# Kernel tuning notes

Measured on AMD Instinct MI355X. Metric: run time of the kernel, lower is better.

The kernel has to match this reference:

```python
import jax, jax.numpy as jnp
import numpy as np

N_LAT, N_LON = 721, 1440
N_MESH = 40962
C_IN, N_FEAT = 64, 4
HID, OUT = 256, 256
BATCH = 2


def _precompute_interp(mesh_lat, mesh_lon):
    """Vectorized version of BilinearInterpolator.__init__ precompute."""
    lat_min, lon_min = -np.pi / 2, 0.0
    dlat = np.pi / (N_LAT - 1)
    dlon = 2 * np.pi / N_LON
    lon = np.mod(mesh_lon - lon_min, 2 * np.pi) + lon_min
    lat_idx = (mesh_lat - lat_min) / dlat
    lon_idx = (lon - lon_min) / dlon
    i0 = np.clip(np.floor(lat_idx).astype(np.int64), 0, N_LAT - 2)
    j0 = np.clip(np.floor(lon_idx).astype(np.int64), 0, N_LON - 2)
    i1 = i0 + 1
    j1 = (j0 + 1) % N_LON
    lf = np.clip(lat_idx - i0, 0.0, 1.0)
    jf = np.clip(lon_idx - j0, 0.0, 1.0)
    idx = np.stack([i0 * N_LON + j0, i0 * N_LON + j1,
                    i1 * N_LON + j0, i1 * N_LON + j1], axis=1)
    w = np.stack([(1 - lf) * (1 - jf), (1 - lf) * jf,
                  lf * (1 - jf), lf * jf], axis=1).astype(np.float32)
    return idx, w


def setup_inputs() -> dict:
    key = jax.random.key(0)
    k = jax.random.split(key, 6)
    rng = np.random.default_rng(0)
    mesh_lat = rng.uniform(-np.pi / 2 + 1e-3, np.pi / 2 - 1e-3, N_MESH)
    mesh_lon = rng.uniform(0.0, 2 * np.pi, N_MESH)
    idx, w = _precompute_interp(mesh_lat, mesh_lon)
    d_in = C_IN + N_FEAT
    return {
        "grid_data": jax.random.normal(k[0], (BATCH, N_LAT, N_LON, C_IN), jnp.float32),
        "mesh_features": jax.random.normal(k[1], (N_MESH, N_FEAT), jnp.float32),
        "indices": jnp.asarray(idx, jnp.int64 if jax.config.read('jax_enable_x64') else jnp.int32),
        "weights": jnp.asarray(w),
        "W1": jax.random.normal(k[2], (d_in, HID), jnp.float32) / np.sqrt(d_in),
        "b1": jnp.zeros((HID,), jnp.float32),
        "W2": jax.random.normal(k[3], (HID, OUT), jnp.float32) / np.sqrt(HID),
        "b2": jnp.zeros((OUT,), jnp.float32),
    }


def reference(grid_data, mesh_features, indices, weights, W1, b1, W2, b2):
    B, n_lat, n_lon, C = grid_data.shape
    grid_flat = grid_data.reshape(B, n_lat * n_lon, C)          # (B, G, C)
    corner = grid_flat[:, indices, :]                           # (B, M, 4, C)
    mesh_data = jnp.einsum('bmkc,mk->bmc', corner, weights)     # weighted 4-pt sum
    mf = jnp.broadcast_to(mesh_features[None], (B,) + mesh_features.shape)
    combined = jnp.concatenate([mesh_data, mf], axis=-1)        # (B, M, C+F)
    h = jax.nn.relu(combined @ W1 + b1)                         # 2-layer MLP
    return h @ W2 + b2                                          # (B, M, OUT)
```

## Files before the change

kernel.cpp:

```cpp
#include <hip/hip_runtime.h>
#include <hip/hip_bf16.h>


constexpr int kNLat  = 721;
constexpr int kNLon  = 1440;
constexpr long long kNPix = (long long)kNLat * kNLon;
constexpr int kMesh  = 40962;
constexpr int kCIn   = 64;
constexpr int kFeat  = 4;
constexpr int kDIn   = kCIn + kFeat;
constexpr int kHid   = 256;
constexpr int kOut   = 256;
constexpr int kBatch = 2;

constexpr int kPts    = kBatch * kMesh;
constexpr int kPtsPad = (kPts + 63) & ~63;

typedef __attribute__((ext_vector_type(8))) short bf16x8;
typedef __attribute__((ext_vector_type(4))) float f32x4;

constexpr int    WSA1_N   = 16 * 3 * 64 * 8;
constexpr int    WSB2_N   = 16 * 8 * 64 * 8;
constexpr size_t WS_BYTES = (size_t)(WSA1_N + WSB2_N) * 2;

constexpr int MP    = 64;
constexpr int NBLKB = kPtsPad / MP;
constexpr int CSTR  = 128;
constexpr int HSTR  = 256;

__device__ inline ushort f2b(float v) {
    __hip_bfloat16 h = __float2bfloat16(v);
    return *reinterpret_cast<ushort*>(&h);
}

__device__ inline int cswz(int r, int c) { return r * CSTR + (c ^ ((r & 7) << 3)); }
__device__ inline int hswz(int r, int c) { return r * HSTR + (c ^ ((r & 7) << 3)); }

__global__ __launch_bounds__(256)
void g2m_prep(const float* __restrict__ W1, const float* __restrict__ W2,
              ushort* __restrict__ ws) {
    const int tid = blockIdx.x * 256 + threadIdx.x;
    if (tid < 3072) {
        const int l  = tid & 63;
        const int g  = tid >> 6;
        const int ks = g % 3;
        const int rt = g / 3;
        const int hid = rt * 16 + (l & 15);
        const int k0  = ks * 32 + (l >> 4) * 8;
        ushort tmp[8];
        #pragma unroll
        for (int j = 0; j < 8; ++j) {
            const int k = k0 + j;
            tmp[j] = f2b(k < kDIn ? W1[(size_t)k * kHid + hid] : 0.f);
        }
        *reinterpret_cast<bf16x8*>(ws + (size_t)tid * 8) =
            *reinterpret_cast<bf16x8*>(tmp);
    } else if (tid < 11264) {
        const int q  = tid - 3072;
        const int l  = q & 63;
        const int g  = q >> 6;
        const int ks = g % 8;
        const int ct = g / 8;
        const int col = ct * 16 + (l & 15);
        const int k0  = ks * 32 + (l >> 4) * 8;
        ushort tmp[8];
        #pragma unroll
        for (int j = 0; j < 8; ++j) {
            const int k = k0 + j;
            tmp[j] = f2b(W2[(size_t)k * kOut + col]);
        }
        *reinterpret_cast<bf16x8*>(ws + (size_t)(WSA1_N + q * 8)) =
            *reinterpret_cast<bf16x8*>(tmp);
    }
}

__global__ __launch_bounds__(256, 3)
void g2m_fused3(const float* __restrict__ grid,
                const float* __restrict__ mfeat,
                const int*   __restrict__ indices,
                const float* __restrict__ weights,
                const float* __restrict__ b1,
                const float* __restrict__ b2,
                const ushort* __restrict__ ws,
                float* __restrict__ out)
{
    __shared__ __align__(16) ushort comb[MP * CSTR];
    __shared__ __align__(16) ushort hbuf[MP * HSTR];

    const int t    = threadIdx.x;
    const int lane = t & 63;
    const int w    = t >> 6;
    const int p0   = blockIdx.x * MP;
    const int l15  = lane & 15;
    const int l4   = lane >> 4;

    {
        const int q = l4;
        float4 rr[4][4];
        float4 wtv[4];
        float  mf0[4], mf1[4];

        #pragma unroll
        for (int it = 0; it < 4; ++it) {
            const int p = p0 + w * 16 + it * 4 + q;
            rr[it][0] = rr[it][1] = rr[it][2] = rr[it][3] = float4{0.f, 0.f, 0.f, 0.f};
            wtv[it] = float4{0.f, 0.f, 0.f, 0.f};
            mf0[it] = 0.f; mf1[it] = 0.f;
            if (p < kPts) {
                const int b = (p >= kMesh) ? 1 : 0;
                const int m = p - b * kMesh;
                const int4 id = *reinterpret_cast<const int4*>(indices + (size_t)m * 4);
                wtv[it] = *reinterpret_cast<const float4*>(weights + (size_t)m * 4);
                const float* gb = grid + (size_t)b * (size_t)(kNPix * kCIn);
                rr[it][0] = *reinterpret_cast<const float4*>(gb + (size_t)id.x * kCIn + l15 * 4);
                rr[it][1] = *reinterpret_cast<const float4*>(gb + (size_t)id.y * kCIn + l15 * 4);
                rr[it][2] = *reinterpret_cast<const float4*>(gb + (size_t)id.z * kCIn + l15 * 4);
                rr[it][3] = *reinterpret_cast<const float4*>(gb + (size_t)id.w * kCIn + l15 * 4);
                if (l15 < 2) {
                    mf0[it] = mfeat[(size_t)m * kFeat + l15 * 2];
                    mf1[it] = mfeat[(size_t)m * kFeat + l15 * 2 + 1];
                }
            }
        }

        #pragma unroll
        for (int it = 0; it < 4; ++it) {
            const int row = w * 16 + it * 4 + q;
            const float4 wt = wtv[it];
            float4 acc;
            acc.x = fmaf(wt.x, rr[it][0].x, fmaf(wt.y, rr[it][1].x, fmaf(wt.z, rr[it][2].x, wt.w * rr[it][3].x)));
            acc.y = fmaf(wt.x, rr[it][0].y, fmaf(wt.y, rr[it][1].y, fmaf(wt.z, rr[it][2].y, wt.w * rr[it][3].y)));
            acc.z = fmaf(wt.x, rr[it][0].z, fmaf(wt.y, rr[it][1].z, fmaf(wt.z, rr[it][2].z, wt.w * rr[it][3].z)));
            acc.w = fmaf(wt.x, rr[it][0].w, fmaf(wt.y, rr[it][1].w, fmaf(wt.z, rr[it][2].w, wt.w * rr[it][3].w)));
            ushort4 pk;
            pk.x = f2b(acc.x); pk.y = f2b(acc.y); pk.z = f2b(acc.z); pk.w = f2b(acc.w);
            *reinterpret_cast<ushort4*>(&comb[cswz(row, l15 * 4)]) = pk;
            ushort2 ft;
            ft.x = f2b(mf0[it]); ft.y = f2b(mf1[it]);
            *reinterpret_cast<ushort2*>(&comb[cswz(row, 64 + l15 * 2)]) = ft;
        }
    }
    __syncthreads();

    {
        f32x4 acc1[4][4];
        #pragma unroll
        for (int r = 0; r < 4; ++r)
            #pragma unroll
            for (int mt = 0; mt < 4; ++mt) acc1[r][mt] = (f32x4)0.f;

        #pragma unroll
        for (int ks = 0; ks < 3; ++ks) {
            bf16x8 af[4], bfr[4];
            #pragma unroll
            for (int r = 0; r < 4; ++r) {
                const int rt = w * 4 + r;
                af[r] = *reinterpret_cast<const bf16x8*>(
                            ws + (size_t)((rt * 3 + ks) * 64 + lane) * 8);
            }
            #pragma unroll
            for (int mt = 0; mt < 4; ++mt)
                bfr[mt] = *reinterpret_cast<const bf16x8*>(
                            &comb[cswz(mt * 16 + l15, ks * 32 + l4 * 8)]);
            #pragma unroll
            for (int r = 0; r < 4; ++r)
                #pragma unroll
                for (int mt = 0; mt < 4; ++mt)
                    acc1[r][mt] = __builtin_amdgcn_mfma_f32_16x16x32_bf16(
                                      af[r], bfr[mt], acc1[r][mt], 0, 0, 0);
        }

        #pragma unroll
        for (int r = 0; r < 4; ++r) {
            const int hid0 = (w * 4 + r) * 16 + l4 * 4;
            const float4 bv = *reinterpret_cast<const float4*>(b1 + hid0);
            #pragma unroll
            for (int mt = 0; mt < 4; ++mt) {
                const int m = mt * 16 + l15;
                ushort4 hv;
                hv.x = f2b(fmaxf(acc1[r][mt][0] + bv.x, 0.f));
                hv.y = f2b(fmaxf(acc1[r][mt][1] + bv.y, 0.f));
                hv.z = f2b(fmaxf(acc1[r][mt][2] + bv.z, 0.f));
                hv.w = f2b(fmaxf(acc1[r][mt][3] + bv.w, 0.f));
                *reinterpret_cast<ushort4*>(&hbuf[hswz(m, hid0)]) = hv;
            }
        }
    }
    __syncthreads();

    {
        f32x4 acc2[4][4];
        #pragma unroll
        for (int mt = 0; mt < 4; ++mt)
            #pragma unroll
            for (int c = 0; c < 4; ++c) acc2[mt][c] = (f32x4)0.f;

        #pragma unroll
        for (int ks = 0; ks < 8; ++ks) {
            bf16x8 hf[4], wf[4];
            #pragma unroll
            for (int mt = 0; mt < 4; ++mt)
                hf[mt] = *reinterpret_cast<const bf16x8*>(
                            &hbuf[hswz(mt * 16 + l15, ks * 32 + l4 * 8)]);
            #pragma unroll
            for (int c = 0; c < 4; ++c) {
                const int ct = w * 4 + c;
                wf[c] = *reinterpret_cast<const bf16x8*>(
                            ws + (size_t)(WSA1_N + ((ct * 8 + ks) * 64 + lane) * 8));
            }
            #pragma unroll
            for (int mt = 0; mt < 4; ++mt)
                #pragma unroll
                for (int c = 0; c < 4; ++c)
                    acc2[mt][c] = __builtin_amdgcn_mfma_f32_16x16x32_bf16(
                                      wf[c], hf[mt], acc2[mt][c], 0, 0, 0);
        }

        #pragma unroll
        for (int c = 0; c < 4; ++c) {
            const int col0 = (w * 4 + c) * 16 + l4 * 4;
            const float4 bv = *reinterpret_cast<const float4*>(b2 + col0);
            #pragma unroll
            for (int mt = 0; mt < 4; ++mt) {
                const int p = p0 + mt * 16 + l15;
                if (p < kPts) {
                    float4 o;
                    o.x = acc2[mt][c][0] + bv.x;
                    o.y = acc2[mt][c][1] + bv.y;
                    o.z = acc2[mt][c][2] + bv.z;
                    o.w = acc2[mt][c][3] + bv.w;
                    *reinterpret_cast<float4*>(out + (size_t)p * kOut + col0) = o;
                }
            }
        }
    }
}

extern "C" void kernel_launch(void* const* d_in, const int* in_sizes, int n_in,
                              void* d_out, int out_size, void* d_ws, size_t ws_size,
                              hipStream_t stream) {
    const float* grid    = (const float*)d_in[0];
    const float* mfeat   = (const float*)d_in[1];
    const int*   indices = (const int*)d_in[2];
    const float* weights = (const float*)d_in[3];
    const float* W1      = (const float*)d_in[4];
    const float* b1      = (const float*)d_in[5];
    const float* W2      = (const float*)d_in[6];
    const float* b2      = (const float*)d_in[7];
    float* o = (float*)d_out;

    if (ws_size >= WS_BYTES) {
        ushort* ws = (ushort*)d_ws;
        g2m_prep<<<44, 256, 0, stream>>>(W1, W2, ws);
        g2m_fused3<<<NBLKB, 256, 0, stream>>>(grid, mfeat, indices, weights,
                                              b1, b2, ws, o);
    }
}
```

Before: 52.88 us.

## Process two point tiles per block, prefetching second gather during first MLP

Each block now handles two 64-point tiles. It loads the index, weight and feature metadata for both tiles up front, then issues the grid-row gather for the second tile while the first tile's two MFMA GEMMs run. A second LDS staging buffer holds the second tile's combined input, and occupancy is lowered from 3 to 2 blocks per CU with half as many blocks launched. The goal is to hide gather latency behind the matrix work. The cost is much higher register pressure from holding a second tile's gathered rows, which could cause spills, plus lower occupancy and an uneven tail across CUs.

```diff
diff --git a/kernel.cpp b/kernel.cpp
--- a/kernel.cpp
+++ b/kernel.cpp
@@ -24,7 +24,7 @@
 constexpr size_t WS_BYTES = (size_t)(WSA1_N + WSB2_N) * 2;
 
 constexpr int MP    = 64;
-constexpr int NBLKB = kPtsPad / MP;
+constexpr int NBLK2 = (kPtsPad + 2 * MP - 1) / (2 * MP);
 constexpr int CSTR  = 128;
 constexpr int HSTR  = 256;
 
@@ -74,8 +74,177 @@
     }
 }
 
-__global__ __launch_bounds__(256, 3)
-void g2m_fused3(const float* __restrict__ grid,
+struct GRegs {
+    float4 rr[4][4];
+    float4 wt[4];
+    float  mf0[4], mf1[4];
+};
+
+__device__ inline void load_meta(const int* __restrict__ indices,
+                                 const float* __restrict__ weights,
+                                 const float* __restrict__ mfeat,
+                                 int p0, int w, int l15, int l4,
+                                 int4 (&id)[4], GRegs& g) {
+    #pragma unroll
+    for (int it = 0; it < 4; ++it) {
+        const int p = p0 + w * 16 + it * 4 + l4;
+        id[it] = int4{0, 0, 0, 0};
+        g.wt[it] = float4{0.f, 0.f, 0.f, 0.f};
+        g.mf0[it] = 0.f; g.mf1[it] = 0.f;
+        if (p < kPts) {
+            const int b = (p >= kMesh) ? 1 : 0;
+            const int m = p - b * kMesh;
+            id[it] = *reinterpret_cast<const int4*>(indices + (size_t)m * 4);
+            id[it].x += b ? (int)kNPix : 0;
+            id[it].y += b ? (int)kNPix : 0;
+            id[it].z += b ? (int)kNPix : 0;
+            id[it].w += b ? (int)kNPix : 0;
+            g.wt[it] = *reinterpret_cast<const float4*>(weights + (size_t)m * 4);
+            if (l15 < 2) {
+                g.mf0[it] = mfeat[(size_t)m * kFeat + l15 * 2];
+                g.mf1[it] = mfeat[(size_t)m * kFeat + l15 * 2 + 1];
+            }
+        }
+    }
+}
+
+__device__ inline void load_rows(const float* __restrict__ grid,
+                                 int p0, int w, int l15, int l4,
+                                 const int4 (&id)[4], GRegs& g) {
+    #pragma unroll
+    for (int it = 0; it < 4; ++it) {
+        const int p = p0 + w * 16 + it * 4 + l4;
+        g.rr[it][0] = g.rr[it][1] = g.rr[it][2] = g.rr[it][3] = float4{0.f, 0.f, 0.f, 0.f};
+        if (p < kPts) {
+            g.rr[it][0] = *reinterpret_cast<const float4*>(grid + (size_t)id[it].x * kCIn + l15 * 4);
+            g.rr[it][1] = *reinterpret_cast<const float4*>(grid + (size_t)id[it].y * kCIn + l15 * 4);
+            g.rr[it][2] = *reinterpret_cast<const float4*>(grid + (size_t)id[it].z * kCIn + l15 * 4);
+            g.rr[it][3] = *reinterpret_cast<const float4*>(grid + (size_t)id[it].w * kCIn + l15 * 4);
+        }
+    }
+}
+
+__device__ inline void reduce_tile(const GRegs& g, ushort* comb,
+                                   int w, int l15, int l4) {
+    #pragma unroll
+    for (int it = 0; it < 4; ++it) {
+        const int row = w * 16 + it * 4 + l4;
+        const float4 wt = g.wt[it];
+        float4 acc;
+        acc.x = fmaf(wt.x, g.rr[it][0].x, fmaf(wt.y, g.rr[it][1].x, fmaf(wt.z, g.rr[it][2].x, wt.w * g.rr[it][3].x)));
+        acc.y = fmaf(wt.x, g.rr[it][0].y, fmaf(wt.y, g.rr[it][1].y, fmaf(wt.z, g.rr[it][2].y, wt.w * g.rr[it][3].y)));
+        acc.z = fmaf(wt.x, g.rr[it][0].z, fmaf(wt.y, g.rr[it][1].z, fmaf(wt.z, g.rr[it][2].z, wt.w * g.rr[it][3].z)));
+        acc.w = fmaf(wt.x, g.rr[it][0].w, fmaf(wt.y, g.rr[it][1].w, fmaf(wt.z, g.rr[it][2].w, wt.w * g.rr[it][3].w)));
+        ushort4 pk;
+        pk.x = f2b(acc.x); pk.y = f2b(acc.y); pk.z = f2b(acc.z); pk.w = f2b(acc.w);
+        *reinterpret_cast<ushort4*>(&comb[cswz(row, l15 * 4)]) = pk;
+        ushort2 ft;
+        ft.x = f2b(g.mf0[it]); ft.y = f2b(g.mf1[it]);
+        *reinterpret_cast<ushort2*>(&comb[cswz(row, 64 + l15 * 2)]) = ft;
+    }
+}
+
+__device__ inline void gemm1(const ushort* comb, ushort* hbuf,
+                             const ushort* __restrict__ ws,
+                             const float* __restrict__ b1,
+                             int w, int lane, int l15, int l4) {
+    f32x4 acc1[4][4];
+    #pragma unroll
+    for (int r = 0; r < 4; ++r)
+        #pragma unroll
+        for (int mt = 0; mt < 4; ++mt) acc1[r][mt] = (f32x4)0.f;
+
+    #pragma unroll
+    for (int ks = 0; ks < 3; ++ks) {
+        bf16x8 af[4], bfr[4];
+        #pragma unroll
+        for (int r = 0; r < 4; ++r) {
+            const int rt = w * 4 + r;
+            af[r] = *reinterpret_cast<const bf16x8*>(
+                        ws + (size_t)((rt * 3 + ks) * 64 + lane) * 8);
+        }
+        #pragma unroll
+        for (int mt = 0; mt < 4; ++mt)
+            bfr[mt] = *reinterpret_cast<const bf16x8*>(
+                        &comb[cswz(mt * 16 + l15, ks * 32 + l4 * 8)]);
+        #pragma unroll
+        for (int r = 0; r < 4; ++r)
+            #pragma unroll
+            for (int mt = 0; mt < 4; ++mt)
+                acc1[r][mt] = __builtin_amdgcn_mfma_f32_16x16x32_bf16(
+                                  af[r], bfr[mt], acc1[r][mt], 0, 0, 0);
+    }
+
+    #pragma unroll
+    for (int r = 0; r < 4; ++r) {
+        const int hid0 = (w * 4 + r) * 16 + l4 * 4;
+        const float4 bv = *reinterpret_cast<const float4*>(b1 + hid0);
+        #pragma unroll
+        for (int mt = 0; mt < 4; ++mt) {
+            const int m = mt * 16 + l15;
+            ushort4 hv;
+            hv.x = f2b(fmaxf(acc1[r][mt][0] + bv.x, 0.f));
+            hv.y = f2b(fmaxf(acc1[r][mt][1] + bv.y, 0.f));
+            hv.z = f2b(fmaxf(acc1[r][mt][2] + bv.z, 0.f));
+            hv.w = f2b(fmaxf(acc1[r][mt][3] + bv.w, 0.f));
+            *reinterpret_cast<ushort4*>(&hbuf[hswz(m, hid0)]) = hv;
+        }
+    }
+}
+
+__device__ inline void gemm2(const ushort* hbuf,
+                             const ushort* __restrict__ ws,
+                             const float* __restrict__ b2,
+                             float* __restrict__ out,
+                             int p0, int w, int lane, int l15, int l4) {
+    f32x4 acc2[4][4];
+    #pragma unroll
+    for (int mt = 0; mt < 4; ++mt)
+        #pragma unroll
+        for (int c = 0; c < 4; ++c) acc2[mt][c] = (f32x4)0.f;
+
+    #pragma unroll
+    for (int ks = 0; ks < 8; ++ks) {
+        bf16x8 hf[4], wf[4];
+        #pragma unroll
+        for (int mt = 0; mt < 4; ++mt)
+            hf[mt] = *reinterpret_cast<const bf16x8*>(
+                        &hbuf[hswz(mt * 16 + l15, ks * 32 + l4 * 8)]);
+        #pragma unroll
+        for (int c = 0; c < 4; ++c) {
+            const int ct = w * 4 + c;
+            wf[c] = *reinterpret_cast<const bf16x8*>(
+                        ws + (size_t)(WSA1_N + ((ct * 8 + ks) * 64 + lane) * 8));
+        }
+        #pragma unroll
+        for (int mt = 0; mt < 4; ++mt)
+            #pragma unroll
+            for (int c = 0; c < 4; ++c)
+                acc2[mt][c] = __builtin_amdgcn_mfma_f32_16x16x32_bf16(
+                                  wf[c], hf[mt], acc2[mt][c], 0, 0, 0);
+    }
+
+    #pragma unroll
+    for (int c = 0; c < 4; ++c) {
+        const int col0 = (w * 4 + c) * 16 + l4 * 4;
+        const float4 bv = *reinterpret_cast<const float4*>(b2 + col0);
+        #pragma unroll
+        for (int mt = 0; mt < 4; ++mt) {
+            const int p = p0 + mt * 16 + l15;
+            if (p < kPts) {
+                float4 o;
+                o.x = acc2[mt][c][0] + bv.x;
+                o.y = acc2[mt][c][1] + bv.y;
+                o.z = acc2[mt][c][2] + bv.z;
+                o.w = acc2[mt][c][3] + bv.w;
+                *reinterpret_cast<float4*>(out + (size_t)p * kOut + col0) = o;
+            }
+        }
+    }
+}
+
+__global__ __launch_bounds__(256, 2)
+void g2m_fused5(const float* __restrict__ grid,
                 const float* __restrict__ mfeat,
                 const int*   __restrict__ indices,
                 const float* __restrict__ weights,
@@ -84,156 +253,40 @@
                 const ushort* __restrict__ ws,
                 float* __restrict__ out)
 {
-    __shared__ __align__(16) ushort comb[MP * CSTR];
+    __shared__ __align__(16) ushort comb0[MP * CSTR];
+    __shared__ __align__(16) ushort comb1[MP * CSTR];
     __shared__ __align__(16) ushort hbuf[MP * HSTR];
 
     const int t    = threadIdx.x;
     const int lane = t & 63;
     const int w    = t >> 6;
-    const int p0   = blockIdx.x * MP;
+    const int pa   = blockIdx.x * (2 * MP);
+    const int pb   = pa + MP;
     const int l15  = lane & 15;
     const int l4   = lane >> 4;
 
-    {
-        const int q = l4;
-        float4 rr[4][4];
-        float4 wtv[4];
-        float  mf0[4], mf1[4];
-
-        #pragma unroll
-        for (int it = 0; it < 4; ++it) {
-            const int p = p0 + w * 16 + it * 4 + q;
-            rr[it][0] = rr[it][1] = rr[it][2] = rr[it][3] = float4{0.f, 0.f, 0.f, 0.f};
-            wtv[it] = float4{0.f, 0.f, 0.f, 0.f};
-            mf0[it] = 0.f; mf1[it] = 0.f;
-            if (p < kPts) {
-                const int b = (p >= kMesh) ? 1 : 0;
-                const int m = p - b * kMesh;
-                const int4 id = *reinterpret_cast<const int4*>(indices + (size_t)m * 4);
-                wtv[it] = *reinterpret_cast<const float4*>(weights + (size_t)m * 4);
-                const float* gb = grid + (size_t)b * (size_t)(kNPix * kCIn);
-                rr[it][0] = *reinterpret_cast<const float4*>(gb + (size_t)id.x * kCIn + l15 * 4);
-                rr[it][1] = *reinterpret_cast<const float4*>(gb + (size_t)id.y * kCIn + l15 * 4);
-                rr[it][2] = *reinterpret_cast<const float4*>(gb + (size_t)id.z * kCIn + l15 * 4);
-                rr[it][3] = *reinterpret_cast<const float4*>(gb + (size_t)id.w * kCIn + l15 * 4);
-                if (l15 < 2) {
-                    mf0[it] = mfeat[(size_t)m * kFeat + l15 * 2];
-                    mf1[it] = mfeat[(size_t)m * kFeat + l15 * 2 + 1];
-                }
-            }
-        }
-
-        #pragma unroll
-        for (int it = 0; it < 4; ++it) {
-            const int row = w * 16 + it * 4 + q;
-            const float4 wt = wtv[it];
-            float4 acc;
-            acc.x = fmaf(wt.x, rr[it][0].x, fmaf(wt.y, rr[it][1].x, fmaf(wt.z, rr[it][2].x, wt.w * rr[it][3].x)));
-            acc.y = fmaf(wt.x, rr[it][0].y, fmaf(wt.y, rr[it][1].y, fmaf(wt.z, rr[it][2].y, wt.w * rr[it][3].y)));
-            acc.z = fmaf(wt.x, rr[it][0].z, fmaf(wt.y, rr[it][1].z, fmaf(wt.z, rr[it][2].z, wt.w * rr[it][3].z)));
-            acc.w = fmaf(wt.x, rr[it][0].w, fmaf(wt.y, rr[it][1].w, fmaf(wt.z, rr[it][2].w, wt.w * rr[it][3].w)));
-            ushort4 pk;
-            pk.x = f2b(acc.x); pk.y = f2b(acc.y); pk.z = f2b(acc.z); pk.w = f2b(acc.w);
-            *reinterpret_cast<ushort4*>(&comb[cswz(row, l15 * 4)]) = pk;
-            ushort2 ft;
-            ft.x = f2b(mf0[it]); ft.y = f2b(mf1[it]);
-            *reinterpret_cast<ushort2*>(&comb[cswz(row, 64 + l15 * 2)]) = ft;
-        }
-    }
+    int4  id0[4], id1[4];
+    GRegs g0, g1;
+
+    load_meta(indices, weights, mfeat, pa, w, l15, l4, id0, g0);
+    load_meta(indices, weights, mfeat, pb, w, l15, l4, id1, g1);
+    load_rows(grid, pa, w, l15, l4, id0, g0);
+
+    reduce_tile(g0, comb0, w, l15, l4);
     __syncthreads();
 
-    {
-        f32x4 acc1[4][4];
-        #pragma unroll
-        for (int r = 0; r < 4; ++r)
-            #pragma unroll
-            for (int mt = 0; mt < 4; ++mt) acc1[r][mt] = (f32x4)0.f;
-
-        #pragma unroll
-        for (int ks = 0; ks < 3; ++ks) {
-            bf16x8 af[4], bfr[4];
-            #pragma unroll
-            for (int r = 0; r < 4; ++r) {
-                const int rt = w * 4 + r;
-                af[r] = *reinterpret_cast<const bf16x8*>(
-                            ws + (size_t)((rt * 3 + ks) * 64 + lane) * 8);
-            }
-            #pragma unroll
-            for (int mt = 0; mt < 4; ++mt)
-                bfr[mt] = *reinterpret_cast<const bf16x8*>(
-                            &comb[cswz(mt * 16 + l15, ks * 32 + l4 * 8)]);
-            #pragma unroll
-            for (int r = 0; r < 4; ++r)
-                #pragma unroll
-                for (int mt = 0; mt < 4; ++mt)
-                    acc1[r][mt] = __builtin_amdgcn_mfma_f32_16x16x32_bf16(
-                                      af[r], bfr[mt], acc1[r][mt], 0, 0, 0);
-        }
-
-        #pragma unroll
-        for (int r = 0; r < 4; ++r) {
-            const int hid0 = (w * 4 + r) * 16 + l4 * 4;
-            const float4 bv = *reinterpret_cast<const float4*>(b1 + hid0);
-            #pragma unroll
-            for (int mt = 0; mt < 4; ++mt) {
-                const int m = mt * 16 + l15;
-                ushort4 hv;
-                hv.x = f2b(fmaxf(acc1[r][mt][0] + bv.x, 0.f));
-                hv.y = f2b(fmaxf(acc1[r][mt][1] + bv.y, 0.f));
-                hv.z = f2b(fmaxf(acc1[r][mt][2] + bv.z, 0.f));
-                hv.w = f2b(fmaxf(acc1[r][mt][3] + bv.w, 0.f));
-                *reinterpret_cast<ushort4*>(&hbuf[hswz(m, hid0)]) = hv;
-            }
-        }
-    }
+    load_rows(grid, pb, w, l15, l4, id1, g1);
+
+    gemm1(comb0, hbuf, ws, b1, w, lane, l15, l4);
     __syncthreads();
-
-    {
-        f32x4 acc2[4][4];
-        #pragma unroll
-        for (int mt = 0; mt < 4; ++mt)
-            #pragma unroll
-            for (int c = 0; c < 4; ++c) acc2[mt][c] = (f32x4)0.f;
-
-        #pragma unroll
-        for (int ks = 0; ks < 8; ++ks) {
-            bf16x8 hf[4], wf[4];
-            #pragma unroll
-            for (int mt = 0; mt < 4; ++mt)
-                hf[mt] = *reinterpret_cast<const bf16x8*>(
-                            &hbuf[hswz(mt * 16 + l15, ks * 32 + l4 * 8)]);
-            #pragma unroll
-            for (int c = 0; c < 4; ++c) {
-                const int ct = w * 4 + c;
-                wf[c] = *reinterpret_cast<const bf16x8*>(
-                            ws + (size_t)(WSA1_N + ((ct * 8 + ks) * 64 + lane) * 8));
-            }
-            #pragma unroll
-            for (int mt = 0; mt < 4; ++mt)
-                #pragma unroll
-                for (int c = 0; c < 4; ++c)
-                    acc2[mt][c] = __builtin_amdgcn_mfma_f32_16x16x32_bf16(
-                                      wf[c], hf[mt], acc2[mt][c], 0, 0, 0);
-        }
-
-        #pragma unroll
-        for (int c = 0; c < 4; ++c) {
-            const int col0 = (w * 4 + c) * 16 + l4 * 4;
-            const float4 bv = *reinterpret_cast<const float4*>(b2 + col0);
-            #pragma unroll
-            for (int mt = 0; mt < 4; ++mt) {
-                const int p = p0 + mt * 16 + l15;
-                if (p < kPts) {
-                    float4 o;
-                    o.x = acc2[mt][c][0] + bv.x;
-                    o.y = acc2[mt][c][1] + bv.y;
-                    o.z = acc2[mt][c][2] + bv.z;
-                    o.w = acc2[mt][c][3] + bv.w;
-                    *reinterpret_cast<float4*>(out + (size_t)p * kOut + col0) = o;
-                }
-            }
-        }
-    }
+    gemm2(hbuf, ws, b2, out, pa, w, lane, l15, l4);
+
+    reduce_tile(g1, comb1, w, l15, l4);
+    __syncthreads();
+
+    gemm1(comb1, hbuf, ws, b1, w, lane, l15, l4);
+    __syncthreads();
+    gemm2(hbuf, ws, b2, out, pb, w, lane, l15, l4);
 }
 
 extern "C" void kernel_launch(void* const* d_in, const int* in_sizes, int n_in,
@@ -252,7 +305,7 @@
     if (ws_size >= WS_BYTES) {
         ushort* ws = (ushort*)d_ws;
         g2m_prep<<<44, 256, 0, stream>>>(W1, W2, ws);
-        g2m_fused3<<<NBLKB, 256, 0, stream>>>(grid, mfeat, indices, weights,
+        g2m_fused5<<<NBLK2, 256, 0, stream>>>(grid, mfeat, indices, weights,
                                               b1, b2, ws, o);
     }
 }
```

Measured after the change: 70.10 us. +32.6%, slower.
